# Kernel tuning notes

Measured on AMD Instinct MI355X. Metric: run time of the kernel, lower is better.

The kernel has to match this reference:

```python
import jax, jax.numpy as jnp
import numpy as np

C = 64      # in_channels
D = 64      # hidden_dim (= per-head out dim since concat=False)
H = 4       # heads
N1 = 20000
N2 = 20000
E = 320000
NEG_SLOPE = 0.2


def setup_inputs() -> dict:
    key = jax.random.key(0)
    ks = jax.random.split(key, 32)
    inp = {}
    inp['x1'] = jax.random.normal(ks[0], (N1, C), dtype=jnp.float32)
    inp['x2'] = jax.random.normal(ks[1], (N2, C), dtype=jnp.float32)
    inp['edge_index1'] = jax.random.randint(ks[2], (2, E), 0, N1, dtype=jnp.int64)
    inp['edge_index2'] = jax.random.randint(ks[3], (2, E), 0, N2, dtype=jnp.int64)
    i = 4
    for tag in ['0', '1', '2', 'f']:
        inp['W' + tag] = jax.random.normal(ks[i], (H * D, C), dtype=jnp.float32) / np.sqrt(C); i += 1
        inp['as' + tag] = jax.random.normal(ks[i], (H, D), dtype=jnp.float32) * 0.1; i += 1
        inp['ad' + tag] = jax.random.normal(ks[i], (H, D), dtype=jnp.float32) * 0.1; i += 1
        inp['b' + tag] = jax.random.normal(ks[i], (C,), dtype=jnp.float32) * 0.02; i += 1
    inp['Wr'] = jax.random.normal(ks[i], (C, C), dtype=jnp.float32) / np.sqrt(C); i += 1
    inp['br'] = jax.random.normal(ks[i], (C,), dtype=jnp.float32) * 0.02
    return inp


def _build_edges(edge_index1, edge_index2, n1, n2):
    """Eval-mode combined edge list: e1 | e2+n1 | e1+n1, coalesced (dedup),
    then self-loops replaced with the full set (PyG GATConv behavior).
    Host-side numpy since edge dedup is data-dependent."""
    e1 = np.asarray(edge_index1)
    e2 = np.asarray(edge_index2) + n1
    e1o = e1 + n1  # edge_manipulator eval path: offset then mask (always valid here)
    valid = (e1o[0] < n1 + n2) & (e1o[1] < n1 + n2)
    e1o = e1o[:, valid]
    comb = np.concatenate([e1, e2, e1o], axis=1)
    comb = np.unique(comb, axis=1)  # coalesce: sort + dedup
    n = n1 + n2
    comb = comb[:, comb[0] != comb[1]]  # remove self loops
    loops = np.arange(n, dtype=comb.dtype)
    src = np.concatenate([comb[0], loops])
    dst = np.concatenate([comb[1], loops])
    return jnp.asarray(src), jnp.asarray(dst)


def gat(h_in, src, dst, n, W, a_s, a_d, b):
    # PyG GATConv, concat=False: mean over heads, bias of size out_channels.
    h = (h_in @ W.T).reshape(n, H, -1)                    # [N,H,D]
    asrc = jnp.einsum('nhd,hd->nh', h, a_s)               # [N,H]
    adst = jnp.einsum('nhd,hd->nh', h, a_d)
    e = jax.nn.leaky_relu(asrc[src] + adst[dst], NEG_SLOPE)  # [E,H]
    m = jax.ops.segment_max(e, dst, num_segments=n)
    ex = jnp.exp(e - m[dst])
    s = jax.ops.segment_sum(ex, dst, num_segments=n)
    alpha = ex / (s[dst] + 1e-16)                         # segment softmax over in-edges
    out = jax.ops.segment_sum(alpha[:, :, None] * h[src], dst, num_segments=n)  # [N,H,D]
    return out.mean(axis=1) + b


def reference(x1, x2, edge_index1, edge_index2,
              W0, as0, ad0, b0, W1, as1, ad1, b1, W2, as2, ad2, b2,
              Wf, asf, adf, bf, Wr, br):
    n1, n2 = x1.shape[0], x2.shape[0]
    n = n1 + n2
    src, dst = _build_edges(edge_index1, edge_index2, n1, n2)

    residual = x2 @ Wr.T + br
    h = jnp.concatenate([x1, x2], axis=0)
    # stacked layers (run under no_grad in torch; same forward math, eval dropout = identity)
    for (W, a_s, a_d, b) in [(W0, as0, ad0, b0), (W1, as1, ad1, b1), (W2, as2, ad2, b2)]:
        h = jax.nn.relu(gat(h, src, dst, n, W, a_s, a_d, b))
    h = gat(h, src, dst, n, Wf, asf, adf, bf)

    h2 = h[n1:n1 + n2]
    norm = jnp.linalg.norm(h2, axis=1, keepdims=True)
    h2n = h2 / jnp.maximum(norm, 1e-12)  # F.normalize(p=2, dim=1)
    return h2n + residual
```

## Files before the change

kernel.cpp:

```cpp
#include <hip/hip_runtime.h>

#define N1V 20000
#define N2V 20000
#define NU  20000
#define NUP 20032
#define EV  320000
#define CAP 128
#define CSTR 16
#define BSTR 272
#define BMW 640

typedef _Float16 f16x8 __attribute__((ext_vector_type(8)));
typedef float    f32x4 __attribute__((ext_vector_type(4)));
typedef float    f32x2 __attribute__((ext_vector_type(2)));

__device__ __forceinline__ unsigned short f2h_bits(float f){
  return __builtin_bit_cast(unsigned short, (_Float16)f);
}

__device__ __forceinline__ unsigned char f2fp8(float f){
#if __has_builtin(__builtin_amdgcn_cvt_pk_fp8_f32)
  int pk = __builtin_amdgcn_cvt_pk_fp8_f32(f, 0.f, 0, false);
  return (unsigned char)(pk & 0xff);
#else
  float a = fabsf(f);
  unsigned sgn = (f < 0.f) ? 0x80u : 0u;
  if (!(a == a)) return (unsigned char)(sgn | 0x7f);
  if (a < 7.8125e-3f) return (unsigned char)sgn;
  if (a > 448.f) a = 448.f;
  unsigned u = __float_as_uint(a);
  int e = (int)((u >> 23) & 0xff) - 127;
  unsigned m = (u >> 20) & 7u;
  unsigned rest = u & 0xfffffu;
  if (rest > 0x80000u || (rest == 0x80000u && (m & 1u))){ m++; if (m == 8u){ m = 0u; e++; } }
  if (e < -6) return (unsigned char)sgn;
  if (e > 8){ e = 8; m = 7u; }
  return (unsigned char)(sgn | ((unsigned)(e + 7) << 3) | m);
#endif
}

template<bool HI>
__device__ __forceinline__ f32x2 fp8pair(unsigned v){
#if __has_builtin(__builtin_amdgcn_cvt_pk_f32_fp8)
  auto t = __builtin_amdgcn_cvt_pk_f32_fp8((int)v, HI);
  return __builtin_bit_cast(f32x2, t);
#else
  unsigned b0 = (v >> (HI ? 16 : 0)) & 0xffu, b1 = (v >> (HI ? 24 : 8)) & 0xffu;
  auto one = [](unsigned b)->float{
    unsigned s = b & 0x80u, ef = (b >> 3) & 15u, m = b & 7u;
    float mag = ef ? __uint_as_float(((ef + 120u) << 23) | (m << 20))
                   : (float)m * 0.001953125f;
    return s ? -mag : mag;
  };
  f32x2 r = {one(b0), one(b1)};
  return r;
#endif
}

__global__ __launch_bounds__(256) void zero_init(unsigned* __restrict__ c1,
                                                 unsigned* __restrict__ c2,
                                                 unsigned* __restrict__ flag){
  int i = blockIdx.x*256 + threadIdx.x;
  if (i < NU*CSTR){ c1[i] = 0u; c2[i] = 0u; }
  if (i == 0) *flag = 0u;
}

__global__ void detect_dtype(const unsigned* __restrict__ e, unsigned* __restrict__ flag){
  unsigned v = e[2*threadIdx.x + 1];
  if (v) atomicOr(flag, 1u);
}

__device__ __forceinline__ int rd_idx(const void* p, long long i, bool is64){
  return is64 ? (int)((const long long*)p)[i] : ((const int*)p)[i];
}

__global__ void scatter_buckets(const void* e1, const void* e2, const unsigned* __restrict__ flag,
                                unsigned* __restrict__ c1, unsigned* __restrict__ c2,
                                unsigned short* __restrict__ bucket){
  int i = blockIdx.x*blockDim.x + threadIdx.x;
  if (i >= 2*EV) return;
  bool is64 = (*flag == 0u);
  if (i < EV){
    int s = rd_idx(e1, i, is64), d = rd_idx(e1, (long long)EV+i, is64);
    if (s != d){
      unsigned p = atomicAdd(&c1[(size_t)d*CSTR], 1u);
      if (p < CAP) bucket[(size_t)d*BSTR + p] = (unsigned short)s;
    }
  } else {
    int j = i - EV;
    int s = rd_idx(e2, j, is64), d = rd_idx(e2, (long long)EV+j, is64);
    if (s != d){
      unsigned p = atomicAdd(&c2[(size_t)d*CSTR], 1u);
      if (p < CAP) bucket[(size_t)d*BSTR + CAP + p] = (unsigned short)s;
    }
  }
}

__global__ __launch_bounds__(256) void dedup_rows(
    unsigned short* __restrict__ bucket,
    const unsigned* __restrict__ c1, const unsigned* __restrict__ c2,
    unsigned* __restrict__ rowcnt)
{
  __shared__ unsigned bm[4][BMW];
  int w = threadIdx.x >> 6, lane = threadIdx.x & 63;
  int t = blockIdx.x*4 + w;
  unsigned* bmw = bm[w];
  #pragma unroll
  for (int i = lane; i < BMW; i += 64) bmw[i] = 0u;
  __syncthreads();

  unsigned a = c1[(size_t)t*CSTR]; if (a > CAP) a = CAP;
  unsigned bb = c2[(size_t)t*CSTR]; if (bb > CAP) bb = CAP;
  int nA = (int)a, nB = (int)bb;
  unsigned short* row = &bucket[(size_t)t*BSTR];
  int cnt = nA + nB;
  int wc = 0;
  for (int i0 = 0; i0 < cnt; i0 += 64){
    int i = i0 + lane;
    bool act = (i < cnt);
    unsigned v = 0u;
    if (act) v = (i < nA) ? (unsigned)row[i] : (unsigned)row[CAP + (i - nA)];
    bool keep = false;
    if (act){
      unsigned bit = 1u << (v & 31u);
      unsigned old = atomicOr(&bmw[v >> 5], bit);
      keep = (old & bit) == 0u;
    }
    unsigned long long mask = __ballot(keep);
    int pos = wc + (int)__popcll(mask & ((1ull << lane) - 1ull));
    if (keep) row[pos] = (unsigned short)v;
    wc += (int)__popcll(mask);
  }
  if (lane == 0){
    row[wc] = (unsigned short)t;
    rowcnt[t] = (unsigned)(wc + 1);
  }
}

__global__ __launch_bounds__(256) void gemm_hp(
    const float* __restrict__ hin, const float* __restrict__ x2,
    const float* __restrict__ W,
    const float* __restrict__ a_s, const float* __restrict__ a_d,
    unsigned char* __restrict__ hp8, float* __restrict__ asv, float* __restrict__ adv)
{
  __shared__ __align__(16) unsigned short As[64][72];
  __shared__ __align__(16) unsigned short Bs[256][72];
  int tid = threadIdx.x;
  int nb  = blockIdx.x * 64;
  for (int i = tid; i < 256*64; i += 256)
    Bs[i>>6][i&63] = f2h_bits(W[i]);
  const float* src = hin ? hin : x2;
  for (int i = tid; i < 64*64; i += 256){
    int r = i>>6, c = i&63;
    int gn = nb + r; if (gn >= NU) gn = NU-1;
    As[r][c] = f2h_bits(src[(size_t)gn*64 + c]);
  }
  __syncthreads();

  int w = tid >> 6, lane = tid & 63;
  int fr = lane & 15, fq = lane >> 4;
  int wc = w * 64;
  const f32x4 zero = {0.f, 0.f, 0.f, 0.f};
  f32x4 acc[4][4];
  #pragma unroll
  for (int a=0; a<4; ++a)
    #pragma unroll
    for (int b=0; b<4; ++b) acc[a][b] = zero;

  #pragma unroll
  for (int ks=0; ks<2; ++ks){
    int k0 = ks*32 + fq*8;
    f16x8 af[4], bfv[4];
    #pragma unroll
    for (int rt=0; rt<4; ++rt) af[rt]  = *(const f16x8*)&As[rt*16 + fr][k0];
    #pragma unroll
    for (int ct=0; ct<4; ++ct) bfv[ct] = *(const f16x8*)&Bs[wc + ct*16 + fr][k0];
    #pragma unroll
    for (int rt=0; rt<4; ++rt)
      #pragma unroll
      for (int ct=0; ct<4; ++ct)
        acc[rt][ct] = __builtin_amdgcn_mfma_f32_16x16x32_f16(af[rt], bfv[ct], acc[rt][ct], 0, 0, 0);
  }

  #pragma unroll
  for (int rt=0; rt<4; ++rt)
    #pragma unroll
    for (int ct=0; ct<4; ++ct)
      #pragma unroll
      for (int j=0; j<4; ++j){
        int gn = nb + rt*16 + fq*4 + j;
        int o  = wc + ct*16 + fr;
        hp8[(size_t)gn*256 + ((o & 63) << 2) + (o >> 6)] = f2fp8(acc[rt][ct][j]);
      }

  float asr[4], adr[4];
  #pragma unroll
  for (int ct=0; ct<4; ++ct){
    asr[ct] = a_s[wc + ct*16 + fr];
    adr[ct] = a_d[wc + ct*16 + fr];
  }
  #pragma unroll
  for (int rt=0; rt<4; ++rt)
    #pragma unroll
    for (int j=0; j<4; ++j){
      float ps = acc[rt][0][j]*asr[0] + acc[rt][1][j]*asr[1]
               + acc[rt][2][j]*asr[2] + acc[rt][3][j]*asr[3];
      float pd = acc[rt][0][j]*adr[0] + acc[rt][1][j]*adr[1]
               + acc[rt][2][j]*adr[2] + acc[rt][3][j]*adr[3];
      #pragma unroll
      for (int off=1; off<16; off<<=1){
        ps += __shfl_xor(ps, off);
        pd += __shfl_xor(pd, off);
      }
      if (fr == 0){
        int gn = nb + rt*16 + fq*4 + j;
        asv[(size_t)gn*4 + w] = ps;
        adv[(size_t)gn*4 + w] = pd;
      }
    }
}

template<int MODE>
__global__ __launch_bounds__(256) void gat_aggr8(
    const unsigned short* __restrict__ bucket, const unsigned* __restrict__ rowcnt,
    const unsigned char* __restrict__ hp8,
    const float* __restrict__ asv, const float* __restrict__ adv,
    const float* __restrict__ bias, float* __restrict__ hout,
    const float* __restrict__ resid, float* __restrict__ outp)
{
  __shared__ __align__(16) float4 wbuf[4][64];
  int w    = threadIdx.x >> 6;
  int lane = threadIdx.x & 63;
  int dst  = blockIdx.x*4 + w;
  const unsigned short* row = &bucket[(size_t)dst*BSTR];
  int cnt = (int)rowcnt[dst];
  float4 adn = *(const float4*)&adv[(size_t)dst*4];
  float4* wrow = wbuf[w];

  f32x2 accA = {0.f, 0.f}, accB = {0.f, 0.f};
  float ss0=0.f, ss1=0.f, ss2=0.f, ss3=0.f;

#define GATHER1(J) { \
    int su = __builtin_amdgcn_readlane(sv, (J)); \
    float4 wv = wrow[(J)]; \
    unsigned hv = *(const unsigned*)(hp8 + (((size_t)(unsigned)su) << 8) + (lane << 2)); \
    f32x2 h01 = fp8pair<false>(hv); \
    f32x2 h23 = fp8pair<true>(hv); \
    f32x2 w01 = {wv.x, wv.y}, w23 = {wv.z, wv.w}; \
    accA += h01 * w01; \
    accB += h23 * w23; }

  for (int i0=0; i0<cnt; i0+=64){
    int i = i0 + lane;
    int sv = 0; float x0=0.f, x1=0.f, x2v=0.f, x3=0.f;
    if (i < cnt){
      sv = (int)row[i];
      float4 a = *(const float4*)&asv[(size_t)sv*4];
      float e0 = a.x + adn.x; e0 = e0 > 0.f ? e0 : 0.2f*e0; x0  = __expf(e0 - 4.f);
      float e1 = a.y + adn.y; e1 = e1 > 0.f ? e1 : 0.2f*e1; x1  = __expf(e1 - 4.f);
      float e2 = a.z + adn.z; e2 = e2 > 0.f ? e2 : 0.2f*e2; x2v = __expf(e2 - 4.f);
      float e3 = a.w + adn.w; e3 = e3 > 0.f ? e3 : 0.2f*e3; x3  = __expf(e3 - 4.f);
      ss0 += x0; ss1 += x1; ss2 += x2v; ss3 += x3;
    }
    float4 wpk = {x0, x1, x2v, x3};
    wrow[lane] = wpk;
    __builtin_amdgcn_wave_barrier();
    int lim = cnt - i0; if (lim > 64) lim = 64;
    int lim8 = (lim + 7) & ~7;
    for (int j = 0; j < lim8; j += 8){
      GATHER1(j)
      GATHER1(j+1)
      GATHER1(j+2)
      GATHER1(j+3)
      GATHER1(j+4)
      GATHER1(j+5)
      GATHER1(j+6)
      GATHER1(j+7)
    }
    __builtin_amdgcn_wave_barrier();
  }
#undef GATHER1

  #pragma unroll
  for (int off=32; off; off>>=1){
    ss0 += __shfl_xor(ss0, off); ss1 += __shfl_xor(ss1, off);
    ss2 += __shfl_xor(ss2, off); ss3 += __shfl_xor(ss3, off);
  }
  float r = 0.25f*( accA.x/(ss0 + 1e-16f) + accA.y/(ss1 + 1e-16f)
                  + accB.x/(ss2 + 1e-16f) + accB.y/(ss3 + 1e-16f) ) + bias[lane];
  if (MODE == 0){
    r = fmaxf(r, 0.f);
    hout[(size_t)dst*64 + lane] = r;
  } else {
    float ssq = r*r;
    #pragma unroll
    for (int off=32; off; off>>=1) ssq += __shfl_xor(ssq, off);
    float sc = 1.f / fmaxf(sqrtf(ssq), 1e-12f);
    size_t o = (size_t)dst*64 + lane;
    outp[o] = r*sc + resid[o];
  }
}

__global__ __launch_bounds__(256) void resid_gemm(const float* __restrict__ x2,
    const float* __restrict__ Wr, const float* __restrict__ br, float* __restrict__ resid){
  __shared__ float WT[64][65];
  int tid = threadIdx.x;
  for (int i = tid; i < 64*64; i += 256) WT[i & 63][i >> 6] = Wr[i];
  __syncthreads();
  int row = blockIdx.x*4 + (tid >> 6);
  int c   = tid & 63;
  const float* xr = &x2[(size_t)row*64];
  float acc = br[c];
  #pragma unroll 8
  for (int k=0; k<64; ++k) acc = fmaf(xr[k], WT[k][c], acc);
  resid[(size_t)row*64 + c] = acc;
}

extern "C" void kernel_launch(void* const* d_in, const int* in_sizes, int n_in,
                              void* d_out, int out_size, void* d_ws, size_t ws_size,
                              hipStream_t stream)
{
  (void)in_sizes; (void)n_in; (void)out_size; (void)ws_size;
  const float* x2  = (const float*)d_in[1];
  const void*  ei1 = d_in[2];
  const void*  ei2 = d_in[3];
  const float* Wm[4] = {(const float*)d_in[4],  (const float*)d_in[8],
                        (const float*)d_in[12], (const float*)d_in[16]};
  const float* Asv[4] = {(const float*)d_in[5],  (const float*)d_in[9],
                         (const float*)d_in[13], (const float*)d_in[17]};
  const float* Adv[4] = {(const float*)d_in[6],  (const float*)d_in[10],
                         (const float*)d_in[14], (const float*)d_in[18]};
  const float* Bv[4]  = {(const float*)d_in[7],  (const float*)d_in[11],
                         (const float*)d_in[15], (const float*)d_in[19]};
  const float* Wr = (const float*)d_in[20];
  const float* br = (const float*)d_in[21];
  float* out = (float*)d_out;

  char* p = (char*)d_ws;
  auto alloc = [&](size_t b){ void* r = (void*)p; p += (b + 1023) & ~(size_t)1023; return r; };
  unsigned* c1      = (unsigned*)alloc((size_t)NU*CSTR*4);
  unsigned* c2      = (unsigned*)alloc((size_t)NU*CSTR*4);
  unsigned* rowcnt  = (unsigned*)alloc((size_t)NU*4);
  unsigned short* bucket = (unsigned short*)alloc((size_t)NU*BSTR*2);
  unsigned char* hp8 = (unsigned char*)alloc((size_t)NUP*256);
  float* asv   = (float*)alloc((size_t)NUP*4*4);
  float* adv   = (float*)alloc((size_t)NUP*4*4);
  float* bufA  = (float*)alloc((size_t)NUP*64*4);
  float* bufB  = (float*)alloc((size_t)NUP*64*4);
  float* resid = (float*)alloc((size_t)N2V*64*4);
  unsigned* flag = (unsigned*)alloc(4);

  zero_init<<<(NU*CSTR + 255)/256, 256, 0, stream>>>(c1, c2, flag);
  detect_dtype<<<1, 256, 0, stream>>>((const unsigned*)ei1, flag);
  scatter_buckets<<<(2*EV + 255)/256, 256, 0, stream>>>(ei1, ei2, flag, c1, c2, bucket);
  dedup_rows<<<NU/4, 256, 0, stream>>>(bucket, c1, c2, rowcnt);
  resid_gemm<<<N2V/4, 256, 0, stream>>>(x2, Wr, br, resid);

  const float* hin = nullptr;
  float* houts[3] = {bufA, bufB, bufA};
  for (int l = 0; l < 3; ++l){
    gemm_hp<<<NUP/64, 256, 0, stream>>>(hin, x2, Wm[l], Asv[l], Adv[l], hp8, asv, adv);
    gat_aggr8<0><<<NU/4, 256, 0, stream>>>(bucket, rowcnt, hp8, asv, adv, Bv[l],
                                           houts[l], nullptr, nullptr);
    hin = houts[l];
  }
  gemm_hp<<<NUP/64, 256, 0, stream>>>(hin, x2, Wm[3], Asv[3], Adv[3], hp8, asv, adv);
  gat_aggr8<2><<<NU/4, 256, 0, stream>>>(bucket, rowcnt, hp8, asv, adv, Bv[3],
                                         nullptr, resid, out);
}
```

Measured before the change: 229.0 us.

## Fuse edge scatter, residual GEMM and first-layer projection into one launch

```diff
diff --git a/kernel.cpp b/kernel.cpp
--- a/kernel.cpp
+++ b/kernel.cpp
@@ -9,6 +9,10 @@
 #define CSTR 16
 #define BSTR 272
 #define BMW 640
+
+#define FB_SC 2500
+#define FB_RS 5000
+#define FB_GM 313
 
 typedef _Float16 f16x8 __attribute__((ext_vector_type(8)));
 typedef float    f32x4 __attribute__((ext_vector_type(4)));
@@ -58,41 +62,138 @@
 }
 
 __global__ __launch_bounds__(256) void zero_init(unsigned* __restrict__ c1,
-                                                 unsigned* __restrict__ c2,
-                                                 unsigned* __restrict__ flag){
+                                                 unsigned* __restrict__ c2){
   int i = blockIdx.x*256 + threadIdx.x;
   if (i < NU*CSTR){ c1[i] = 0u; c2[i] = 0u; }
-  if (i == 0) *flag = 0u;
 }
 
 __global__ void detect_dtype(const unsigned* __restrict__ e, unsigned* __restrict__ flag){
   unsigned v = e[2*threadIdx.x + 1];
-  if (v) atomicOr(flag, 1u);
+  unsigned long long m = __ballot(v != 0u);
+  if (threadIdx.x == 0) *flag = (m != 0ull) ? 1u : 0u;
 }
 
 __device__ __forceinline__ int rd_idx(const void* p, long long i, bool is64){
   return is64 ? (int)((const long long*)p)[i] : ((const int*)p)[i];
 }
 
-__global__ void scatter_buckets(const void* e1, const void* e2, const unsigned* __restrict__ flag,
-                                unsigned* __restrict__ c1, unsigned* __restrict__ c2,
-                                unsigned short* __restrict__ bucket){
-  int i = blockIdx.x*blockDim.x + threadIdx.x;
-  if (i >= 2*EV) return;
-  bool is64 = (*flag == 0u);
-  if (i < EV){
-    int s = rd_idx(e1, i, is64), d = rd_idx(e1, (long long)EV+i, is64);
-    if (s != d){
-      unsigned p = atomicAdd(&c1[(size_t)d*CSTR], 1u);
-      if (p < CAP) bucket[(size_t)d*BSTR + p] = (unsigned short)s;
-    }
+__global__ __launch_bounds__(256) void fused3(
+    const void* __restrict__ e1, const void* __restrict__ e2,
+    const unsigned* __restrict__ flag,
+    unsigned* __restrict__ c1, unsigned* __restrict__ c2,
+    unsigned short* __restrict__ bucket,
+    const float* __restrict__ x2, const float* __restrict__ Wr,
+    const float* __restrict__ br, float* __restrict__ resid,
+    const float* __restrict__ W0, const float* __restrict__ a_s,
+    const float* __restrict__ a_d, unsigned char* __restrict__ hp8,
+    float* __restrict__ asv, float* __restrict__ adv)
+{
+  __shared__ __align__(16) unsigned char smem[46080];
+  int b = blockIdx.x;
+  int tid = threadIdx.x;
+
+  if (b < FB_SC){
+    int i = b*256 + tid;
+    bool is64 = (*flag == 0u);
+    if (i < EV){
+      int s = rd_idx(e1, i, is64), d = rd_idx(e1, (long long)EV+i, is64);
+      if (s != d){
+        unsigned p = atomicAdd(&c1[(size_t)d*CSTR], 1u);
+        if (p < CAP) bucket[(size_t)d*BSTR + p] = (unsigned short)s;
+      }
+    } else {
+      int j = i - EV;
+      int s = rd_idx(e2, j, is64), d = rd_idx(e2, (long long)EV+j, is64);
+      if (s != d){
+        unsigned p = atomicAdd(&c2[(size_t)d*CSTR], 1u);
+        if (p < CAP) bucket[(size_t)d*BSTR + CAP + p] = (unsigned short)s;
+      }
+    }
+  } else if (b < FB_SC + FB_RS){
+    float (*WT)[65] = (float(*)[65])smem;
+    for (int i = tid; i < 64*64; i += 256) WT[i & 63][i >> 6] = Wr[i];
+    __syncthreads();
+    int row = (b - FB_SC)*4 + (tid >> 6);
+    int c   = tid & 63;
+    const float* xr = &x2[(size_t)row*64];
+    float acc = br[c];
+    #pragma unroll 8
+    for (int k=0; k<64; ++k) acc = fmaf(xr[k], WT[k][c], acc);
+    resid[(size_t)row*64 + c] = acc;
   } else {
-    int j = i - EV;
-    int s = rd_idx(e2, j, is64), d = rd_idx(e2, (long long)EV+j, is64);
-    if (s != d){
-      unsigned p = atomicAdd(&c2[(size_t)d*CSTR], 1u);
-      if (p < CAP) bucket[(size_t)d*BSTR + CAP + p] = (unsigned short)s;
-    }
+    unsigned short (*As)[72] = (unsigned short(*)[72])smem;
+    unsigned short (*Bs)[72] = (unsigned short(*)[72])(smem + 9216);
+    int nb = (b - FB_SC - FB_RS) * 64;
+    for (int i = tid; i < 256*64; i += 256)
+      Bs[i>>6][i&63] = f2h_bits(W0[i]);
+    for (int i = tid; i < 64*64; i += 256){
+      int r = i>>6, c = i&63;
+      int gn = nb + r; if (gn >= NU) gn = NU-1;
+      As[r][c] = f2h_bits(x2[(size_t)gn*64 + c]);
+    }
+    __syncthreads();
+
+    int w = tid >> 6, lane = tid & 63;
+    int fr = lane & 15, fq = lane >> 4;
+    int wc = w * 64;
+    const f32x4 zero = {0.f, 0.f, 0.f, 0.f};
+    f32x4 acc[4][4];
+    #pragma unroll
+    for (int a=0; a<4; ++a)
+      #pragma unroll
+      for (int bb=0; bb<4; ++bb) acc[a][bb] = zero;
+
+    #pragma unroll
+    for (int ks=0; ks<2; ++ks){
+      int k0 = ks*32 + fq*8;
+      f16x8 af[4], bfv[4];
+      #pragma unroll
+      for (int rt=0; rt<4; ++rt) af[rt]  = *(const f16x8*)&As[rt*16 + fr][k0];
+      #pragma unroll
+      for (int ct=0; ct<4; ++ct) bfv[ct] = *(const f16x8*)&Bs[wc + ct*16 + fr][k0];
+      #pragma unroll
+      for (int rt=0; rt<4; ++rt)
+        #pragma unroll
+        for (int ct=0; ct<4; ++ct)
+          acc[rt][ct] = __builtin_amdgcn_mfma_f32_16x16x32_f16(af[rt], bfv[ct], acc[rt][ct], 0, 0, 0);
+    }
+
+    #pragma unroll
+    for (int rt=0; rt<4; ++rt)
+      #pragma unroll
+      for (int ct=0; ct<4; ++ct)
+        #pragma unroll
+        for (int j=0; j<4; ++j){
+          int gn = nb + rt*16 + fq*4 + j;
+          int o  = wc + ct*16 + fr;
+          hp8[(size_t)gn*256 + ((o & 63) << 2) + (o >> 6)] = f2fp8(acc[rt][ct][j]);
+        }
+
+    float asr[4], adr[4];
+    #pragma unroll
+    for (int ct=0; ct<4; ++ct){
+      asr[ct] = a_s[wc + ct*16 + fr];
+      adr[ct] = a_d[wc + ct*16 + fr];
+    }
+    #pragma unroll
+    for (int rt=0; rt<4; ++rt)
+      #pragma unroll
+      for (int j=0; j<4; ++j){
+        float ps = acc[rt][0][j]*asr[0] + acc[rt][1][j]*asr[1]
+                 + acc[rt][2][j]*asr[2] + acc[rt][3][j]*asr[3];
+        float pd = acc[rt][0][j]*adr[0] + acc[rt][1][j]*adr[1]
+                 + acc[rt][2][j]*adr[2] + acc[rt][3][j]*adr[3];
+        #pragma unroll
+        for (int off=1; off<16; off<<=1){
+          ps += __shfl_xor(ps, off);
+          pd += __shfl_xor(pd, off);
+        }
+        if (fr == 0){
+          int gn = nb + rt*16 + fq*4 + j;
+          asv[(size_t)gn*4 + w] = ps;
+          adv[(size_t)gn*4 + w] = pd;
+        }
+      }
   }
 }
 
@@ -138,7 +239,7 @@
 }
 
 __global__ __launch_bounds__(256) void gemm_hp(
-    const float* __restrict__ hin, const float* __restrict__ x2,
+    const float* __restrict__ hin,
     const float* __restrict__ W,
     const float* __restrict__ a_s, const float* __restrict__ a_d,
     unsigned char* __restrict__ hp8, float* __restrict__ asv, float* __restrict__ adv)
@@ -149,11 +250,10 @@
   int nb  = blockIdx.x * 64;
   for (int i = tid; i < 256*64; i += 256)
     Bs[i>>6][i&63] = f2h_bits(W[i]);
-  const float* src = hin ? hin : x2;
   for (int i = tid; i < 64*64; i += 256){
     int r = i>>6, c = i&63;
     int gn = nb + r; if (gn >= NU) gn = NU-1;
-    As[r][c] = f2h_bits(src[(size_t)gn*64 + c]);
+    As[r][c] = f2h_bits(hin[(size_t)gn*64 + c]);
   }
   __syncthreads();
 
@@ -266,8 +366,8 @@
     wrow[lane] = wpk;
     __builtin_amdgcn_wave_barrier();
     int lim = cnt - i0; if (lim > 64) lim = 64;
-    int lim8 = (lim + 7) & ~7;
-    for (int j = 0; j < lim8; j += 8){
+    int lim16 = (lim + 15) & ~15;
+    for (int j = 0; j < lim16; j += 16){
       GATHER1(j)
       GATHER1(j+1)
       GATHER1(j+2)
@@ -276,6 +376,14 @@
       GATHER1(j+5)
       GATHER1(j+6)
       GATHER1(j+7)
+      GATHER1(j+8)
+      GATHER1(j+9)
+      GATHER1(j+10)
+      GATHER1(j+11)
+      GATHER1(j+12)
+      GATHER1(j+13)
+      GATHER1(j+14)
+      GATHER1(j+15)
     }
     __builtin_amdgcn_wave_barrier();
   }
@@ -299,21 +407,6 @@
     size_t o = (size_t)dst*64 + lane;
     outp[o] = r*sc + resid[o];
   }
-}
-
-__global__ __launch_bounds__(256) void resid_gemm(const float* __restrict__ x2,
-    const float* __restrict__ Wr, const float* __restrict__ br, float* __restrict__ resid){
-  __shared__ float WT[64][65];
-  int tid = threadIdx.x;
-  for (int i = tid; i < 64*64; i += 256) WT[i & 63][i >> 6] = Wr[i];
-  __syncthreads();
-  int row = blockIdx.x*4 + (tid >> 6);
-  int c   = tid & 63;
-  const float* xr = &x2[(size_t)row*64];
-  float acc = br[c];
-  #pragma unroll 8
-  for (int k=0; k<64; ++k) acc = fmaf(xr[k], WT[k][c], acc);
-  resid[(size_t)row*64 + c] = acc;
 }
 
 extern "C" void kernel_launch(void* const* d_in, const int* in_sizes, int n_in,
@@ -350,21 +443,23 @@
   float* resid = (float*)alloc((size_t)N2V*64*4);
   unsigned* flag = (unsigned*)alloc(4);
 
-  zero_init<<<(NU*CSTR + 255)/256, 256, 0, stream>>>(c1, c2, flag);
-  detect_dtype<<<1, 256, 0, stream>>>((const unsigned*)ei1, flag);
-  scatter_buckets<<<(2*EV + 255)/256, 256, 0, stream>>>(ei1, ei2, flag, c1, c2, bucket);
+  zero_init<<<(NU*CSTR + 255)/256, 256, 0, stream>>>(c1, c2);
+  detect_dtype<<<1, 64, 0, stream>>>((const unsigned*)ei1, flag);
+  fused3<<<FB_SC + FB_RS + FB_GM, 256, 0, stream>>>(
+      ei1, ei2, flag, c1, c2, bucket,
+      x2, Wr, br, resid,
+      Wm[0], Asv[0], Adv[0], hp8, asv, adv);
   dedup_rows<<<NU/4, 256, 0, stream>>>(bucket, c1, c2, rowcnt);
-  resid_gemm<<<N2V/4, 256, 0, stream>>>(x2, Wr, br, resid);
-
-  const float* hin = nullptr;
-  float* houts[3] = {bufA, bufB, bufA};
-  for (int l = 0; l < 3; ++l){
-    gemm_hp<<<NUP/64, 256, 0, stream>>>(hin, x2, Wm[l], Asv[l], Adv[l], hp8, asv, adv);
-    gat_aggr8<0><<<NU/4, 256, 0, stream>>>(bucket, rowcnt, hp8, asv, adv, Bv[l],
-                                           houts[l], nullptr, nullptr);
-    hin = houts[l];
-  }
-  gemm_hp<<<NUP/64, 256, 0, stream>>>(hin, x2, Wm[3], Asv[3], Adv[3], hp8, asv, adv);
+
+  gat_aggr8<0><<<NU/4, 256, 0, stream>>>(bucket, rowcnt, hp8, asv, adv, Bv[0],
+                                         bufA, nullptr, nullptr);
+  gemm_hp<<<NUP/64, 256, 0, stream>>>(bufA, Wm[1], Asv[1], Adv[1], hp8, asv, adv);
+  gat_aggr8<0><<<NU/4, 256, 0, stream>>>(bucket, rowcnt, hp8, asv, adv, Bv[1],
+                                         bufB, nullptr, nullptr);
+  gemm_hp<<<NUP/64, 256, 0, stream>>>(bufB, Wm[2], Asv[2], Adv[2], hp8, asv, adv);
+  gat_aggr8<0><<<NU/4, 256, 0, stream>>>(bucket, rowcnt, hp8, asv, adv, Bv[2],
+                                         bufA, nullptr, nullptr);
+  gemm_hp<<<NUP/64, 256, 0, stream>>>(bufA, Wm[3], Asv[3], Adv[3], hp8, asv, adv);
   gat_aggr8<2><<<NU/4, 256, 0, stream>>>(bucket, rowcnt, hp8, asv, adv, Bv[3],
                                          nullptr, resid, out);
 }
```

Result: slower. 245.3 us (+7.1%).
